# Performance work log

Measured on AMD Instinct MI355X. Metric: run time of the kernel, lower is better.

The kernel has to match this reference:

```python
import jax, jax.numpy as jnp
import numpy as np

DIM = 1024
N_HEADS = 16
HEAD_DIM = DIM // N_HEADS
SCALE = HEAD_DIM ** -0.5


def setup_inputs() -> dict:
    key = jax.random.key(0)
    kx, kq, kk, kv = jax.random.split(key, 4)
    x = jax.random.normal(kx, (2, 2048, DIM), dtype=jnp.float32)
    bv_q = jax.random.normal(kq, (N_HEADS, HEAD_DIM), dtype=jnp.float32) * 0.02
    bv_k = jax.random.normal(kk, (N_HEADS, HEAD_DIM), dtype=jnp.float32) * 0.02
    bv_v = jax.random.normal(kv, (N_HEADS, HEAD_DIM), dtype=jnp.float32) * 0.02
    return {"x": x, "bv_q": bv_q, "bv_k": bv_k, "bv_v": bv_v}


def reference(x, bv_q, bv_k, bv_v):
    B, T, D = x.shape
    H, HD = N_HEADS, HEAD_DIM
    x_h = x.reshape(B, T, H, HD)
    # sign-gated Q/K/V (sign of binding vectors; elementwise +/-1 gating)
    Q = x_h * jnp.sign(bv_q)  # [B,T,H,HD]
    K = x_h * jnp.sign(bv_k)
    V = x_h * jnp.sign(bv_v)
    # causal scores, sigmoid gating (no softmax)
    scores = jnp.einsum('bqhd,bkhd->bhqk', Q, K) * SCALE  # [B,H,T,T]
    causal = jnp.tril(jnp.ones((T, T), dtype=bool))
    attn = jnp.where(causal, jax.nn.sigmoid(scores * 4.0), 0.0)
    out = jnp.einsum('bhqk,bkhd->bqhd', attn, V)  # [B,T,H,HD]
    return out.reshape(B, T, D)
```

## Files before the change

### kernel.cpp

```cpp
#include <hip/hip_runtime.h>
#include <hip/hip_bf16.h>
#include <stdint.h>

#define DIM 1024
#define T_LEN 2048
#define NB 2
#define NH 16
#define HD 64
#define NQT 32

typedef float f32x2 __attribute__((ext_vector_type(2)));
typedef float f32x4 __attribute__((ext_vector_type(4)));
typedef float f32x16 __attribute__((ext_vector_type(16)));
typedef __bf16 bf16x8 __attribute__((ext_vector_type(8)));
typedef __bf16 bf16x2 __attribute__((ext_vector_type(2)));
typedef unsigned int u32;
typedef unsigned int u32x4 __attribute__((ext_vector_type(4)));

template <int N> struct ICT { static constexpr int v = N; };

#define TK(qt, lo, cnt, dst) ((u32)((qt) | ((lo) << 6) | ((cnt) << 12) | ((dst) << 18)))
__constant__ u32 TASKS[80] = {
    TK(31,0,16,1), TK(31,16,16,2), TK(30,15,16,2), TK(15,0,16,0),
    TK(30,0,15,1), TK(29,0,15,1),  TK(29,15,15,2), TK(28,14,15,2), TK(14,0,15,0),
    TK(28,0,14,1), TK(27,0,14,1),  TK(27,14,14,2), TK(26,13,14,2), TK(13,0,14,0),
    TK(26,0,13,1), TK(25,0,13,1),  TK(25,13,13,2), TK(24,12,13,2), TK(12,0,13,0),
    TK(24,0,12,1), TK(23,0,12,1),  TK(23,12,12,2), TK(22,11,12,2), TK(11,0,12,0),
    TK(22,0,11,1), TK(21,0,11,1),  TK(21,11,11,2), TK(20,10,11,2), TK(10,0,11,0),
    TK(20,0,10,1), TK(19,0,10,1),  TK(19,10,10,2), TK(18,9,10,2),  TK(9,0,10,0),
    TK(18,0,9,1),  TK(17,0,9,1),   TK(17,9,9,2),   TK(16,8,9,2),   TK(8,0,9,0),
    TK(16,0,8,1),  TK(7,0,8,0),
    TK(6,0,7,0), TK(5,0,6,0), TK(4,0,5,0), TK(3,0,4,0),
    TK(2,0,3,0), TK(1,0,2,0), TK(0,0,1,0),
    TK(31,0,32,0), TK(30,0,31,0), TK(29,0,30,0), TK(28,0,29,0),
    TK(27,0,28,0), TK(26,0,27,0), TK(25,0,26,0), TK(24,0,25,0),
    TK(23,0,24,0), TK(22,0,23,0), TK(21,0,22,0), TK(20,0,21,0),
    TK(19,0,20,0), TK(18,0,19,0), TK(17,0,18,0), TK(16,0,17,0),
    TK(15,0,16,0), TK(14,0,15,0), TK(13,0,14,0), TK(12,0,13,0),
    TK(11,0,12,0), TK(10,0,11,0), TK(9,0,10,0),  TK(8,0,9,0),
    TK(7,0,8,0),   TK(6,0,7,0),   TK(5,0,6,0),   TK(4,0,5,0),
    TK(3,0,4,0),   TK(2,0,3,0),   TK(1,0,2,0),   TK(0,0,1,0),
};
#define NSPLIT 48

__device__ __forceinline__ float sgnf(float v) {
    return (v > 0.f) ? 1.f : ((v < 0.f) ? -1.f : 0.f);
}

__device__ __forceinline__ void gload16(const __bf16* g, __bf16* l) {
    __builtin_amdgcn_global_load_lds(
        (__attribute__((address_space(1))) void*)g,
        (__attribute__((address_space(3))) void*)l,
        16, 0, 0);
}

__global__ __launch_bounds__(256) void prep_kernel(
    const float* __restrict__ x, const float* __restrict__ bvq,
    const float* __restrict__ bvk, const float* __restrict__ bvv,
    __bf16* __restrict__ xb, __bf16* __restrict__ xq, __bf16* __restrict__ xt)
{
    __shared__ __align__(16) __bf16 tile[64][72];

    const int bid = blockIdx.x;
    const int h = bid & 15, tmp = bid >> 4, tt = tmp & 31, b = tmp >> 5;
    const int tid = threadIdx.x;
    const int r = tid >> 2, c0 = (tid & 3) * 16;

    const size_t rowbase = ((size_t)(b * T_LEN + tt * 64 + r)) * DIM + h * HD + c0;
    const float* xp = x + rowbase;

    float f[16];
    #pragma unroll
    for (int i = 0; i < 16; i += 4) {
        f32x4 v4 = *(const f32x4*)(xp + i);
        #pragma unroll
        for (int j = 0; j < 4; ++j) f[i + j] = v4[j];
    }
    bf16x8 s0, s1, g0, g1;
    #pragma unroll
    for (int j = 0; j < 8; ++j) {
        s0[j] = (__bf16)f[j];
        s1[j] = (__bf16)f[8 + j];
        float gq0 = sgnf(bvq[h * HD + c0 + j])     * sgnf(bvk[h * HD + c0 + j]);
        float gq1 = sgnf(bvq[h * HD + c0 + 8 + j]) * sgnf(bvk[h * HD + c0 + 8 + j]);
        g0[j] = (__bf16)(f[j] * gq0);
        g1[j] = (__bf16)(f[8 + j] * gq1);
    }
    *(bf16x8*)(xb + rowbase)     = s0;
    *(bf16x8*)(xb + rowbase + 8) = s1;
    *(bf16x8*)(xq + rowbase)     = g0;
    *(bf16x8*)(xq + rowbase + 8) = g1;
    *(bf16x8*)&tile[r][c0]     = s0;
    *(bf16x8*)&tile[r][c0 + 8] = s1;

    __syncthreads();

    const int d = tid >> 2, t0c = (tid & 3) * 16;
    const float g = sgnf(bvv[h * HD + d]);
    __bf16 ov[16];
    #pragma unroll
    for (int i = 0; i < 16; ++i) ov[i] = (__bf16)((float)tile[t0c + i][d] * g);
    bf16x8 o0, o1;
    #pragma unroll
    for (int j = 0; j < 8; ++j) { o0[j] = ov[j]; o1[j] = ov[8 + j]; }
    const size_t obase = ((size_t)((b * NH + h) * HD + d)) * T_LEN + tt * 64 + t0c;
    *(bf16x8*)(xt + obase)     = o0;
    *(bf16x8*)(xt + obase + 8) = o1;
}

__global__ __launch_bounds__(256, 4) void mba_main(
    const __bf16* __restrict__ xq, const __bf16* __restrict__ xb,
    const __bf16* __restrict__ xt,
    float* __restrict__ out, float* __restrict__ ws2, int tbase)
{
    __shared__ __align__(16) __bf16 Kb[3][64][64];
    __shared__ __align__(16) __bf16 Vb[2][64][64];

    const int bid = blockIdx.x;
    const u32 tk = TASKS[tbase + (bid >> 5)];
    const int qt  = tk & 63;
    const int lo  = (tk >> 6) & 63;
    const int CL  = (tk >> 12) & 63;
    const int dst = tk >> 18;

    const int bh = bid & 31;
    const int b = bh >> 4, h = bh & 15;
    const int q0 = qt * 64;

    const int tid = threadIdx.x;
    const int w = tid >> 6, l = tid & 63;
    const int c = l & 31, hi = l >> 5;
    const int qh = w & 1, sh = w >> 1;

    const size_t xb_bh = (size_t)b * T_LEN * DIM + h * HD;
    const size_t xt_bh = (size_t)((b * NH + h) * HD) * T_LEN;

    const int rr = l >> 3;
    const int sw = ((l & 7) ^ rr) << 3;

    const __bf16* kst = xb + xb_bh + (size_t)(lo * 64 + w * 8 + rr) * DIM + sw;
    const __bf16* vst = xt + xt_bh + (size_t)(w * 8 + rr) * T_LEN + lo * 64 + sw;
    const size_t KROW32 = (size_t)32 * DIM;
    const size_t VROW32 = (size_t)32 * T_LEN;
    const size_t KTILE  = (size_t)64 * DIM;

    gload16(kst,          &Kb[0][w * 8][0]);
    gload16(kst + KROW32, &Kb[0][w * 8 + 32][0]);
    gload16(vst,          &Vb[0][w * 8][0]);
    gload16(vst + VROW32, &Vb[0][w * 8 + 32][0]);
    if (CL >= 2) {
        gload16(kst + KTILE,          &Kb[1][w * 8][0]);
        gload16(kst + KTILE + KROW32, &Kb[1][w * 8 + 32][0]);
    }
    kst += 2 * KTILE;
    vst += 64;

    bf16x8 qa[4];
    {
        const __bf16* qp = xq + xb_bh + (size_t)(q0 + qh * 32 + c) * DIM + hi * 8;
        #pragma unroll
        for (int m = 0; m < 4; ++m)
            qa[m] = *(const bf16x8*)(qp + m * 16);
    }

    f32x16 o[2];
    #pragma unroll
    for (int nd = 0; nd < 2; ++nd)
        #pragma unroll
        for (int i = 0; i < 16; ++i) o[nd][i] = 0.f;

    const int krow = sh * 32 + c;
    const int swz = (c & 7) << 4;

    auto body = [&](int lt, auto kbT, auto vbT) {
        constexpr int KB = decltype(kbT)::v;
        constexpr int VB = decltype(vbT)::v;
        const bool last = (lt == CL - 1);
        const bool diag = (lo + lt == qt);
        if (last) { asm volatile("s_waitcnt vmcnt(0)" ::: "memory"); }
        else      { asm volatile("s_waitcnt vmcnt(2)" ::: "memory"); }
        __builtin_amdgcn_sched_barrier(0);
        __builtin_amdgcn_s_barrier();
        __builtin_amdgcn_sched_barrier(0);

        if (lt + 1 < CL) {
            gload16(vst,          &Vb[VB ^ 1][w * 8][0]);
            gload16(vst + VROW32, &Vb[VB ^ 1][w * 8 + 32][0]);
            vst += 64;
        }
        __builtin_amdgcn_sched_barrier(0);
        if (lt + 2 < CL) {
            gload16(kst,          &Kb[(KB + 2) % 3][w * 8][0]);
            gload16(kst + KROW32, &Kb[(KB + 2) % 3][w * 8 + 32][0]);
            kst += KTILE;
        }
        __builtin_amdgcn_sched_barrier(0);

        f32x16 ss;
        #pragma unroll
        for (int i = 0; i < 16; ++i) ss[i] = 0.f;
        #pragma unroll
        for (int m = 0; m < 4; ++m) {
            bf16x8 kf = *(const bf16x8*)((const char*)&Kb[KB][krow][0]
                          + ((m * 32 + hi * 16) ^ swz));
            ss = __builtin_amdgcn_mfma_f32_32x32x16_bf16(kf, qa[m], ss, 0, 0, 0);
        }

        u32 W[8];
        #pragma unroll
        for (int i = 0; i < 8; ++i) {
            const int r0 = 2 * i;
            f32x2 z; z.x = ss[r0]; z.y = ss[r0 + 1];
            z = z * (-0.72134752f);
            f32x2 e;
            e.x = __builtin_amdgcn_exp2f(z.x);
            e.y = __builtin_amdgcn_exp2f(z.y);
            e = e + 1.0f;
            float p0 = __builtin_amdgcn_rcpf(e.x);
            float p1 = __builtin_amdgcn_rcpf(e.y);
            if (diag) {
                const int sl = (r0 & 3) + 8 * (r0 >> 2) + 4 * hi;
                const int sg = sh * 32 + sl;
                const int qg = qh * 32 + c;
                if (sg > qg)     p0 = 0.f;
                if (sg + 1 > qg) p1 = 0.f;
            }
            asm("v_cvt_pk_bf16_f32 %0, %1, %2" : "=v"(W[i]) : "v"(p0), "v"(p1));
        }

        asm volatile("v_permlane32_swap_b32 %0, %1" : "+v"(W[0]), "+v"(W[2]));
        asm volatile("v_permlane32_swap_b32 %0, %1" : "+v"(W[1]), "+v"(W[3]));
        asm volatile("v_permlane32_swap_b32 %0, %1" : "+v"(W[4]), "+v"(W[6]));
        asm volatile("v_permlane32_swap_b32 %0, %1" : "+v"(W[5]), "+v"(W[7]));
        bf16x8 pa0 = __builtin_bit_cast(bf16x8, (u32x4){W[0], W[1], W[2], W[3]});
        bf16x8 pa1 = __builtin_bit_cast(bf16x8, (u32x4){W[4], W[5], W[6], W[7]});

        #pragma unroll
        for (int m = 0; m < 2; ++m) {
            const bf16x8 paM = m ? pa1 : pa0;
            #pragma unroll
            for (int nd = 0; nd < 2; ++nd) {
                bf16x8 vf = *(const bf16x8*)((const char*)&Vb[VB][nd * 32 + c][0]
                              + ((sh * 64 + m * 32 + hi * 16) ^ swz));
                o[nd] = __builtin_amdgcn_mfma_f32_32x32x16_bf16(paM, vf, o[nd], 0, 0, 0);
            }
        }
    };

    for (int t = 0; t < CL; t += 6) {
        body(t, ICT<0>{}, ICT<0>{});
        if (t + 1 < CL) body(t + 1, ICT<1>{}, ICT<1>{});
        if (t + 2 < CL) body(t + 2, ICT<2>{}, ICT<0>{});
        if (t + 3 < CL) body(t + 3, ICT<0>{}, ICT<1>{});
        if (t + 4 < CL) body(t + 4, ICT<1>{}, ICT<0>{});
        if (t + 5 < CL) body(t + 5, ICT<2>{}, ICT<1>{});
    }

    __syncthreads();
    float (*osc)[64] = (float(*)[64]) & Kb[0][0][0];

    if (sh == 1) {
        #pragma unroll
        for (int r = 0; r < 16; ++r) {
            const int qloc = (r & 3) + 8 * (r >> 2) + 4 * hi;
            osc[qh * 32 + qloc][c]      = o[0][r];
            osc[qh * 32 + qloc][32 + c] = o[1][r];
        }
    }
    __syncthreads();
    if (sh == 0) {
        if (dst == 0) {
            #pragma unroll
            for (int r = 0; r < 16; ++r) {
                const int qloc = (r & 3) + 8 * (r >> 2) + 4 * hi;
                const size_t row = (size_t)(b * T_LEN + q0 + qh * 32 + qloc) * DIM + h * HD;
                out[row + c]      = o[0][r] + osc[qh * 32 + qloc][c];
                out[row + 32 + c] = o[1][r] + osc[qh * 32 + qloc][32 + c];
            }
        } else {
            float* wp = ws2 + (size_t)((((qt - 16) * 32 + bh) * 2) + (dst - 1)) * 4096;
            #pragma unroll
            for (int r = 0; r < 16; ++r) {
                const int qloc = (r & 3) + 8 * (r >> 2) + 4 * hi;
                const int qrow = qh * 32 + qloc;
                wp[qrow * 64 + c]      = o[0][r] + osc[qrow][c];
                wp[qrow * 64 + 32 + c] = o[1][r] + osc[qrow][32 + c];
            }
        }
    }
}

__global__ __launch_bounds__(256) void reduce_kernel(
    const float* __restrict__ ws2, float* __restrict__ out)
{
    const int bid = blockIdx.x;
    const int tile = bid >> 2, q4 = bid & 3;
    const int qtw = tile >> 5, bh = tile & 31;
    const int b = bh >> 4, h = bh & 15;

    const float* pa = ws2 + (size_t)((qtw * 32 + bh) * 2) * 4096;
    const float* pb = pa + 4096;

    const int e = q4 * 1024 + threadIdx.x * 4;
    const int qr = e >> 6, d = e & 63;

    f32x4 va = *(const f32x4*)(pa + e);
    f32x4 vb = *(const f32x4*)(pb + e);
    f32x4 s = va + vb;
    *(f32x4*)(out + (size_t)(b * T_LEN + (16 + qtw) * 64 + qr) * DIM + h * HD + d) = s;
}

__global__ __launch_bounds__(256) void mba_fallback(
    const float* __restrict__ x,
    const float* __restrict__ bvq,
    const float* __restrict__ bvk,
    const float* __restrict__ bvv,
    float* __restrict__ out)
{
    __shared__ __align__(16) __bf16 Kb[64][72];
    __shared__ __align__(16) __bf16 Vt[HD][72];
    __shared__ __align__(16) __bf16 Pb[4][16][72];

    const int bid = blockIdx.x;
    const int qt  = (NQT - 1) - (bid & (NQT - 1));
    const int bh  = bid >> 5;
    const int b   = bh >> 4;
    const int h   = bh & 15;

    const int tid = threadIdx.x;
    const int w   = tid >> 6;
    const int l   = tid & 63;
    const int lq  = l & 15;
    const int lh  = l >> 4;

    const int  q0    = qt * 64;
    const long xbase = ((long)b * T_LEN) * DIM + h * HD;

    bf16x8 qa[2];
    {
        const int   qrow = q0 + w * 16 + lq;
        const float* qp  = x + xbase + (long)qrow * DIM + lh * 8;
        const float* gp  = bvq + h * HD + lh * 8;
        #pragma unroll
        for (int ks = 0; ks < 2; ++ks)
            #pragma unroll
            for (int j = 0; j < 8; ++j)
                qa[ks][j] = (__bf16)(qp[ks * 32 + j] * sgnf(gp[ks * 32 + j]));
    }

    f32x4 o[4];
    #pragma unroll
    for (int n = 0; n < 4; ++n) o[n] = (f32x4){0.f, 0.f, 0.f, 0.f};

    const int r_st = tid >> 2;
    const int c0   = (tid & 3) * 16;
    const float* gk = bvk + h * HD + c0;
    const float* gv = bvv + h * HD + c0;

    for (int kvt = 0; kvt <= qt; ++kvt) {
        const int kv0 = kvt * 64;
        __syncthreads();
        {
            const float* kp = x + xbase + (long)(kv0 + r_st) * DIM + c0;
            __bf16 kb[16];
            #pragma unroll
            for (int i = 0; i < 16; ++i) kb[i] = (__bf16)(kp[i] * sgnf(gk[i]));
            *(bf16x8*)&Kb[r_st][c0]     = *(bf16x8*)&kb[0];
            *(bf16x8*)&Kb[r_st][c0 + 8] = *(bf16x8*)&kb[8];
            #pragma unroll
            for (int i = 0; i < 16; ++i)
                Vt[c0 + i][r_st] = (__bf16)(kp[i] * sgnf(gv[i]));
        }
        __syncthreads();

        f32x4 s[4];
        #pragma unroll
        for (int n = 0; n < 4; ++n) s[n] = (f32x4){0.f, 0.f, 0.f, 0.f};
        #pragma unroll
        for (int ks = 0; ks < 2; ++ks)
            #pragma unroll
            for (int n = 0; n < 4; ++n) {
                bf16x8 kf = *(const bf16x8*)&Kb[n * 16 + lq][ks * 32 + lh * 8];
                s[n] = __builtin_amdgcn_mfma_f32_16x16x32_bf16(qa[ks], kf, s[n], 0, 0, 0);
            }

        const bool diag = (kvt == qt);
        #pragma unroll
        for (int n = 0; n < 4; ++n)
            #pragma unroll
            for (int j = 0; j < 4; ++j) {
                float sc = s[n][j];
                float p = __builtin_amdgcn_rcpf(
                              1.f + __builtin_amdgcn_exp2f(-0.72134752f * sc));
                if (diag && (n * 16 + lq) > (w * 16 + lh * 4 + j)) p = 0.f;
                Pb[w][lh * 4 + j][n * 16 + lq] = (__bf16)p;
            }

        #pragma unroll
        for (int ks = 0; ks < 2; ++ks) {
            bf16x8 pf = *(const bf16x8*)&Pb[w][lq][ks * 32 + lh * 8];
            #pragma unroll
            for (int n = 0; n < 4; ++n) {
                bf16x8 vf = *(const bf16x8*)&Vt[n * 16 + lq][ks * 32 + lh * 8];
                o[n] = __builtin_amdgcn_mfma_f32_16x16x32_bf16(pf, vf, o[n], 0, 0, 0);
            }
        }
    }

    float* op = out + ((long)b * T_LEN + q0 + w * 16) * DIM + h * HD;
    #pragma unroll
    for (int n = 0; n < 4; ++n)
        #pragma unroll
        for (int j = 0; j < 4; ++j)
            op[(long)(lh * 4 + j) * DIM + n * 16 + lq] = o[n][j];
}

extern "C" void kernel_launch(void* const* d_in, const int* in_sizes, int n_in,
                              void* d_out, int out_size, void* d_ws, size_t ws_size,
                              hipStream_t stream) {
    (void)in_sizes; (void)n_in; (void)out_size;
    const float* x   = (const float*)d_in[0];
    const float* bvq = (const float*)d_in[1];
    const float* bvk = (const float*)d_in[2];
    const float* bvv = (const float*)d_in[3];
    float* out = (float*)d_out;

    const size_t XB_BYTES = (size_t)NB * T_LEN * DIM * sizeof(__bf16);
    const size_t XQ_BYTES = XB_BYTES;
    const size_t XT_BYTES = XB_BYTES;
    const size_t W2_BYTES = (size_t)16 * 32 * 2 * 4096 * sizeof(float);

    if (ws_size < XB_BYTES + XQ_BYTES + XT_BYTES) {
        mba_fallback<<<NB * NH * NQT, 256, 0, stream>>>(x, bvq, bvk, bvv, out);
        return;
    }

    __bf16* xb = (__bf16*)d_ws;
    __bf16* xq = xb + (size_t)NB * T_LEN * DIM;
    __bf16* xt = xq + (size_t)NB * T_LEN * DIM;

    prep_kernel<<<NB * NQT * NH, 256, 0, stream>>>(x, bvq, bvk, bvv, xb, xq, xt);

    if (ws_size >= XB_BYTES + XQ_BYTES + XT_BYTES + W2_BYTES) {
        float* ws2 = (float*)((char*)d_ws + XB_BYTES + XQ_BYTES + XT_BYTES);
        mba_main<<<NSPLIT * 32, 256, 0, stream>>>(xq, xb, xt, out, ws2, 0);
        reduce_kernel<<<2048, 256, 0, stream>>>(ws2, out);
    } else {
        mba_main<<<32 * 32, 256, 0, stream>>>(xq, xb, xt, out, nullptr, 48);
    }
}
```

Before: 50.46 us.

## Replace split-KV task table and reduce pass with serpentine q-tile ordering

Drops the 48-task split-KV scheme, its workspace partials and the separate reduce kernel. Each block now processes one full causal q-tile, and q-tiles are assigned in a serpentine order within groups of 8 to balance load. It also raises wave priority around the MFMA sections with s_setprio. This removes one kernel launch and the workspace round-trip, but long tiles are no longer split, so the tail of the schedule may become less balanced.

```diff
diff --git a/kernel.cpp b/kernel.cpp
--- a/kernel.cpp
+++ b/kernel.cpp
@@ -19,30 +19,6 @@
 
 template <int N> struct ICT { static constexpr int v = N; };
 
-#define TK(qt, lo, cnt, dst) ((u32)((qt) | ((lo) << 6) | ((cnt) << 12) | ((dst) << 18)))
-__constant__ u32 TASKS[80] = {
-    TK(31,0,16,1), TK(31,16,16,2), TK(30,15,16,2), TK(15,0,16,0),
-    TK(30,0,15,1), TK(29,0,15,1),  TK(29,15,15,2), TK(28,14,15,2), TK(14,0,15,0),
-    TK(28,0,14,1), TK(27,0,14,1),  TK(27,14,14,2), TK(26,13,14,2), TK(13,0,14,0),
-    TK(26,0,13,1), TK(25,0,13,1),  TK(25,13,13,2), TK(24,12,13,2), TK(12,0,13,0),
-    TK(24,0,12,1), TK(23,0,12,1),  TK(23,12,12,2), TK(22,11,12,2), TK(11,0,12,0),
-    TK(22,0,11,1), TK(21,0,11,1),  TK(21,11,11,2), TK(20,10,11,2), TK(10,0,11,0),
-    TK(20,0,10,1), TK(19,0,10,1),  TK(19,10,10,2), TK(18,9,10,2),  TK(9,0,10,0),
-    TK(18,0,9,1),  TK(17,0,9,1),   TK(17,9,9,2),   TK(16,8,9,2),   TK(8,0,9,0),
-    TK(16,0,8,1),  TK(7,0,8,0),
-    TK(6,0,7,0), TK(5,0,6,0), TK(4,0,5,0), TK(3,0,4,0),
-    TK(2,0,3,0), TK(1,0,2,0), TK(0,0,1,0),
-    TK(31,0,32,0), TK(30,0,31,0), TK(29,0,30,0), TK(28,0,29,0),
-    TK(27,0,28,0), TK(26,0,27,0), TK(25,0,26,0), TK(24,0,25,0),
-    TK(23,0,24,0), TK(22,0,23,0), TK(21,0,22,0), TK(20,0,21,0),
-    TK(19,0,20,0), TK(18,0,19,0), TK(17,0,18,0), TK(16,0,17,0),
-    TK(15,0,16,0), TK(14,0,15,0), TK(13,0,14,0), TK(12,0,13,0),
-    TK(11,0,12,0), TK(10,0,11,0), TK(9,0,10,0),  TK(8,0,9,0),
-    TK(7,0,8,0),   TK(6,0,7,0),   TK(5,0,6,0),   TK(4,0,5,0),
-    TK(3,0,4,0),   TK(2,0,3,0),   TK(1,0,2,0),   TK(0,0,1,0),
-};
-#define NSPLIT 48
-
 __device__ __forceinline__ float sgnf(float v) {
     return (v > 0.f) ? 1.f : ((v < 0.f) ? -1.f : 0.f);
 }
@@ -110,22 +86,19 @@
 
 __global__ __launch_bounds__(256, 4) void mba_main(
     const __bf16* __restrict__ xq, const __bf16* __restrict__ xb,
-    const __bf16* __restrict__ xt,
-    float* __restrict__ out, float* __restrict__ ws2, int tbase)
+    const __bf16* __restrict__ xt, float* __restrict__ out)
 {
     __shared__ __align__(16) __bf16 Kb[3][64][64];
     __shared__ __align__(16) __bf16 Vb[2][64][64];
 
     const int bid = blockIdx.x;
-    const u32 tk = TASKS[tbase + (bid >> 5)];
-    const int qt  = tk & 63;
-    const int lo  = (tk >> 6) & 63;
-    const int CL  = (tk >> 12) & 63;
-    const int dst = tk >> 18;
-
+    const int u = bid >> 5;
+    const int jj = u >> 3, aa = u & 7;
+    const int qt = 8 * jj + ((jj & 1) ? (7 - aa) : aa);
     const int bh = bid & 31;
     const int b = bh >> 4, h = bh & 15;
     const int q0 = qt * 64;
+    const int CL = qt + 1;
 
     const int tid = threadIdx.x;
     const int w = tid >> 6, l = tid & 63;
@@ -138,8 +111,8 @@
     const int rr = l >> 3;
     const int sw = ((l & 7) ^ rr) << 3;
 
-    const __bf16* kst = xb + xb_bh + (size_t)(lo * 64 + w * 8 + rr) * DIM + sw;
-    const __bf16* vst = xt + xt_bh + (size_t)(w * 8 + rr) * T_LEN + lo * 64 + sw;
+    const __bf16* kst = xb + xb_bh + (size_t)(w * 8 + rr) * DIM + sw;
+    const __bf16* vst = xt + xt_bh + (size_t)(w * 8 + rr) * T_LEN + sw;
     const size_t KROW32 = (size_t)32 * DIM;
     const size_t VROW32 = (size_t)32 * T_LEN;
     const size_t KTILE  = (size_t)64 * DIM;
@@ -176,7 +149,6 @@
         constexpr int KB = decltype(kbT)::v;
         constexpr int VB = decltype(vbT)::v;
         const bool last = (lt == CL - 1);
-        const bool diag = (lo + lt == qt);
         if (last) { asm volatile("s_waitcnt vmcnt(0)" ::: "memory"); }
         else      { asm volatile("s_waitcnt vmcnt(2)" ::: "memory"); }
         __builtin_amdgcn_sched_barrier(0);
@@ -199,12 +171,14 @@
         f32x16 ss;
         #pragma unroll
         for (int i = 0; i < 16; ++i) ss[i] = 0.f;
+        __builtin_amdgcn_s_setprio(1);
         #pragma unroll
         for (int m = 0; m < 4; ++m) {
             bf16x8 kf = *(const bf16x8*)((const char*)&Kb[KB][krow][0]
                           + ((m * 32 + hi * 16) ^ swz));
             ss = __builtin_amdgcn_mfma_f32_32x32x16_bf16(kf, qa[m], ss, 0, 0, 0);
         }
+        __builtin_amdgcn_s_setprio(0);
 
         u32 W[8];
         #pragma unroll
@@ -218,7 +192,7 @@
             e = e + 1.0f;
             float p0 = __builtin_amdgcn_rcpf(e.x);
             float p1 = __builtin_amdgcn_rcpf(e.y);
-            if (diag) {
+            if (last) {
                 const int sl = (r0 & 3) + 8 * (r0 >> 2) + 4 * hi;
                 const int sg = sh * 32 + sl;
                 const int qg = qh * 32 + c;
@@ -235,6 +209,7 @@
         bf16x8 pa0 = __builtin_bit_cast(bf16x8, (u32x4){W[0], W[1], W[2], W[3]});
         bf16x8 pa1 = __builtin_bit_cast(bf16x8, (u32x4){W[4], W[5], W[6], W[7]});
 
+        __builtin_amdgcn_s_setprio(1);
         #pragma unroll
         for (int m = 0; m < 2; ++m) {
             const bf16x8 paM = m ? pa1 : pa0;
@@ -245,6 +220,7 @@
                 o[nd] = __builtin_amdgcn_mfma_f32_32x32x16_bf16(paM, vf, o[nd], 0, 0, 0);
             }
         }
+        __builtin_amdgcn_s_setprio(0);
     };
 
     for (int t = 0; t < CL; t += 6) {
@@ -269,45 +245,14 @@
     }
     __syncthreads();
     if (sh == 0) {
-        if (dst == 0) {
-            #pragma unroll
-            for (int r = 0; r < 16; ++r) {
-                const int qloc = (r & 3) + 8 * (r >> 2) + 4 * hi;
-                const size_t row = (size_t)(b * T_LEN + q0 + qh * 32 + qloc) * DIM + h * HD;
-                out[row + c]      = o[0][r] + osc[qh * 32 + qloc][c];
-                out[row + 32 + c] = o[1][r] + osc[qh * 32 + qloc][32 + c];
-            }
-        } else {
-            float* wp = ws2 + (size_t)((((qt - 16) * 32 + bh) * 2) + (dst - 1)) * 4096;
-            #pragma unroll
-            for (int r = 0; r < 16; ++r) {
-                const int qloc = (r & 3) + 8 * (r >> 2) + 4 * hi;
-                const int qrow = qh * 32 + qloc;
-                wp[qrow * 64 + c]      = o[0][r] + osc[qrow][c];
-                wp[qrow * 64 + 32 + c] = o[1][r] + osc[qrow][32 + c];
-            }
-        }
-    }
-}
-
-__global__ __launch_bounds__(256) void reduce_kernel(
-    const float* __restrict__ ws2, float* __restrict__ out)
-{
-    const int bid = blockIdx.x;
-    const int tile = bid >> 2, q4 = bid & 3;
-    const int qtw = tile >> 5, bh = tile & 31;
-    const int b = bh >> 4, h = bh & 15;
-
-    const float* pa = ws2 + (size_t)((qtw * 32 + bh) * 2) * 4096;
-    const float* pb = pa + 4096;
-
-    const int e = q4 * 1024 + threadIdx.x * 4;
-    const int qr = e >> 6, d = e & 63;
-
-    f32x4 va = *(const f32x4*)(pa + e);
-    f32x4 vb = *(const f32x4*)(pb + e);
-    f32x4 s = va + vb;
-    *(f32x4*)(out + (size_t)(b * T_LEN + (16 + qtw) * 64 + qr) * DIM + h * HD + d) = s;
+        #pragma unroll
+        for (int r = 0; r < 16; ++r) {
+            const int qloc = (r & 3) + 8 * (r >> 2) + 4 * hi;
+            const size_t row = (size_t)(b * T_LEN + q0 + qh * 32 + qloc) * DIM + h * HD;
+            out[row + c]      = o[0][r] + osc[qh * 32 + qloc][c];
+            out[row + 32 + c] = o[1][r] + osc[qh * 32 + qloc][32 + c];
+        }
+    }
 }
 
 __global__ __launch_bounds__(256) void mba_fallback(
@@ -428,7 +373,6 @@
     const size_t XB_BYTES = (size_t)NB * T_LEN * DIM * sizeof(__bf16);
     const size_t XQ_BYTES = XB_BYTES;
     const size_t XT_BYTES = XB_BYTES;
-    const size_t W2_BYTES = (size_t)16 * 32 * 2 * 4096 * sizeof(float);
 
     if (ws_size < XB_BYTES + XQ_BYTES + XT_BYTES) {
         mba_fallback<<<NB * NH * NQT, 256, 0, stream>>>(x, bvq, bvk, bvv, out);
@@ -440,12 +384,5 @@
     __bf16* xt = xq + (size_t)NB * T_LEN * DIM;
 
     prep_kernel<<<NB * NQT * NH, 256, 0, stream>>>(x, bvq, bvk, bvv, xb, xq, xt);
-
-    if (ws_size >= XB_BYTES + XQ_BYTES + XT_BYTES + W2_BYTES) {
-        float* ws2 = (float*)((char*)d_ws + XB_BYTES + XQ_BYTES + XT_BYTES);
-        mba_main<<<NSPLIT * 32, 256, 0, stream>>>(xq, xb, xt, out, ws2, 0);
-        reduce_kernel<<<2048, 256, 0, stream>>>(ws2, out);
-    } else {
-        mba_main<<<32 * 32, 256, 0, stream>>>(xq, xb, xt, out, nullptr, 48);
-    }
-}
+    mba_main<<<NB * NH * NQT, 256, 0, stream>>>(xq, xb, xt, out);
+}
```

Measured after the change: 47.90 us. 1.05x faster.
